# Kernel optimization log

Measured on AMD Instinct MI355X. Metric: run time of the kernel, lower is better.

The kernel has to match this reference:

```python
import jax, jax.numpy as jnp
import numpy as np

N = 50000      # total nodes
E = 600000     # edges
F_IN = 128     # dataset.num_features
G = 500        # graphs (100 nodes each)
K = 30         # sort-pool k
D1, D2, D3 = 64, 64, 1
DTOT = D1 + D2 + D3  # 129


def gcn_conv(x, W, b, src, dst, dinv, n):
    # PyG GCNConv: x' = D^-1/2 (A+I) D^-1/2 (x W) + b ; src/dst include self-loops
    h = x @ W
    norm = dinv[src] * dinv[dst]
    msg = h[src] * norm[:, None]
    return jax.ops.segment_sum(msg, dst, num_segments=n) + b


def setup_inputs():
    key = jax.random.key(0)
    ks = jax.random.split(key, 24)
    rn = lambda k, s, sc=0.1: jax.random.normal(k, s, dtype=jnp.float32) * sc
    return {
        "x": jax.random.normal(ks[0], (N, F_IN), dtype=jnp.float32),
        "edge_index": jax.random.randint(ks[1], (2, E), 0, N),
        "W1": rn(ks[2], (F_IN, D1)), "b1": rn(ks[3], (D1,)),
        "W2": rn(ks[4], (D1, D2)),  "b2": rn(ks[5], (D2,)),
        "W3": rn(ks[6], (D2, D3)),  "b3": rn(ks[7], (D3,)),
        "Ws1": rn(ks[8], (D1, 1)),  "bs1": rn(ks[9], (1,)),
        "Ws2": rn(ks[10], (D2, 1)), "bs2": rn(ks[11], (1,)),
        "Ws3": rn(ks[12], (D3, 1)), "bs3": rn(ks[13], (1,)),
        "Wc1": rn(ks[14], (16, 1, DTOT)), "bc1": rn(ks[15], (16,)),
        "Wc2": rn(ks[16], (32, 16, 5)),   "bc2": rn(ks[17], (32,)),
        "Wl1": rn(ks[18], (128, 352)),    "bl1": rn(ks[19], (128,)),
        "Wl2": rn(ks[20], (1, 128)),      "bl2": rn(ks[21], (1,)),
        "num_graphs": G,
    }


def reference(x, edge_index, W1, b1, W2, b2, W3, b3, Ws1, bs1, Ws2, bs2, Ws3, bs3,
              Wc1, bc1, Wc2, bc2, Wl1, bl1, Wl2, bl2, num_graphs):
    n = x.shape[0]
    loops = jnp.arange(n)
    src = jnp.concatenate([edge_index[0], loops])
    dst = jnp.concatenate([edge_index[1], loops])
    deg = jnp.zeros((n,), jnp.float32).at[dst].add(1.0)
    dinv = jnp.where(deg > 0, deg ** -0.5, 0.0)

    h = jax.nn.relu(gcn_conv(x, W1, b1, src, dst, dinv, n))
    x1 = gcn_conv(h, Ws1, bs1, src, dst, dinv, n) * h
    h = jax.nn.relu(gcn_conv(h, W2, b2, src, dst, dinv, n))
    x2 = gcn_conv(h, Ws2, bs2, src, dst, dinv, n) * h
    h = jax.nn.relu(gcn_conv(h, W3, b3, src, dst, dinv, n))
    x3 = gcn_conv(h, Ws3, bs3, src, dst, dinv, n) * h
    feats = jnp.concatenate([x1, x2, x3], axis=1)  # [N, 129]

    # global_sort_pool: equal-size graphs (batch = id // npg), sort desc by last channel, keep top-K
    npg = n // num_graphs
    fg = feats.reshape(num_graphs, npg, DTOT)
    order = jnp.argsort(-fg[:, :, -1], axis=1)[:, :K]                 # [G, K]
    pooled = jnp.take_along_axis(fg, order[:, :, None], axis=1)       # [G, K, 129]

    # Conv1d(1->16, kernel=129, stride=129) == per-position dense over the 129-dim blocks
    c1 = jax.nn.relu(jnp.einsum('gkd,cd->gck', pooled, Wc1[:, 0, :]) + bc1[None, :, None])  # [G,16,30]
    mp = c1.reshape(num_graphs, 16, K // 2, 2).max(axis=-1)           # MaxPool1d(2,2) -> [G,16,15]
    c2 = jax.lax.conv_general_dilated(mp, Wc2, window_strides=(1,), padding='VALID',
                                      dimension_numbers=('NCH', 'OIH', 'NCH')) + bc2[None, :, None]
    c2 = jax.nn.relu(c2)                                              # [G,32,11]
    flat = c2.reshape(num_graphs, -1)                                 # [G,352]
    hdd = jax.nn.relu(flat @ Wl1.T + bl1)
    out = hdd @ Wl2.T + bl2
    return out[:, 0]
```

## Files before the change

kernel.cpp:

```cpp
#include <hip/hip_runtime.h>
#include <hip/hip_bf16.h>

#define NN 50000
#define EE 600000
#define FIN 128
#define GG 500
#define NPG 100
#define KK 30
#define SCHUNK 1024

__global__ void psg_deg(const int* __restrict__ dst, int* __restrict__ deg, int e) {
    int i = blockIdx.x * blockDim.x + threadIdx.x;
    if (i < e) atomicAdd(&deg[dst[i]], 1);
}

__global__ __launch_bounds__(SCHUNK) void psg_scan1(const int* __restrict__ deg,
                                                    int* __restrict__ rowptr,
                                                    int* __restrict__ csums,
                                                    float* __restrict__ dinv, int n) {
    __shared__ int sm[SCHUNK];
    int t = threadIdx.x;
    int base = blockIdx.x * SCHUNK;
    int v = (base + t < n) ? deg[base + t] : 0;
    sm[t] = v;
    __syncthreads();
    for (int off = 1; off < SCHUNK; off <<= 1) {
        int u = (t >= off) ? sm[t - off] : 0;
        __syncthreads();
        sm[t] += u;
        __syncthreads();
    }
    if (base + t < n) {
        rowptr[base + t] = sm[t] - v;
        dinv[base + t] = 1.0f / sqrtf((float)(v + 1));
    }
    if (t == SCHUNK - 1) csums[blockIdx.x] = sm[t];
}

__global__ void psg_scan2(int* __restrict__ csums, int nb) {
    int t = threadIdx.x;
    int v = (t < nb) ? csums[t] : 0;
    int x = v;
#pragma unroll
    for (int off = 1; off < 64; off <<= 1) {
        int u = __shfl_up(x, off, 64);
        if (t >= off) x += u;
    }
    if (t < nb) csums[t] = x - v;
}

__global__ __launch_bounds__(SCHUNK) void psg_scan3(int* __restrict__ rowptr,
                                                    int* __restrict__ rowfill,
                                                    const int* __restrict__ csums,
                                                    int n, int e) {
    int i = blockIdx.x * SCHUNK + threadIdx.x;
    if (i < n) {
        int v = rowptr[i] + csums[blockIdx.x];
        rowptr[i] = v;
        rowfill[i] = v;
    }
    if (i == 0) rowptr[n] = e;
}

__global__ void psg_build(const int* __restrict__ src, const int* __restrict__ dst,
                          int* __restrict__ rowfill, int* __restrict__ csr_src, int e) {
    int i = blockIdx.x * blockDim.x + threadIdx.x;
    if (i < e) {
        int pos = atomicAdd(&rowfill[dst[i]], 1);
        csr_src[pos] = src[i];
    }
}

template <int KD>
__global__ __launch_bounds__(256) void psg_gemm(const float* __restrict__ X,
                                                const float* __restrict__ W,
                                                const float* __restrict__ dinv,
                                                float* __restrict__ hs, int n) {
    __shared__ __align__(16) float Xl[16][KD];
    __shared__ __align__(16) float WtF[(KD / 4) * 64 * 4];
    int t = threadIdx.x;
    int r0 = blockIdx.x * 16;
    for (int i = t; i < KD * 64; i += 256) {
        int k = i >> 6, j = i & 63;
        WtF[(((k >> 2) * 64 + j) << 2) + (k & 3)] = W[i];
    }
    for (int i4 = t; i4 < 16 * (KD / 4); i4 += 256) {
        int r = i4 / (KD / 4), u = i4 % (KD / 4);
        int row = r0 + r;
        float4 v = make_float4(0.f, 0.f, 0.f, 0.f);
        if (row < n) v = ((const float4*)(X + (size_t)row * KD))[u];
        ((float4*)&Xl[r][0])[u] = v;
    }
    __syncthreads();
    int j = t & 63, q = t >> 6;
    const float4* Wt4 = (const float4*)WtF;
    float a0 = 0.f, a1 = 0.f, a2 = 0.f, a3 = 0.f;
#pragma unroll 4
    for (int u = 0; u < KD / 4; ++u) {
        float4 wv = Wt4[u * 64 + j];
        float4 x0 = *(const float4*)&Xl[q * 4 + 0][u * 4];
        float4 x1 = *(const float4*)&Xl[q * 4 + 1][u * 4];
        float4 x2 = *(const float4*)&Xl[q * 4 + 2][u * 4];
        float4 x3 = *(const float4*)&Xl[q * 4 + 3][u * 4];
        a0 += x0.x * wv.x + x0.y * wv.y + x0.z * wv.z + x0.w * wv.w;
        a1 += x1.x * wv.x + x1.y * wv.y + x1.z * wv.z + x1.w * wv.w;
        a2 += x2.x * wv.x + x2.y * wv.y + x2.z * wv.z + x2.w * wv.w;
        a3 += x3.x * wv.x + x3.y * wv.y + x3.z * wv.z + x3.w * wv.w;
    }
    float av[4] = {a0, a1, a2, a3};
#pragma unroll
    for (int rr = 0; rr < 4; rr++) {
        int row = r0 + q * 4 + rr;
        if (row < n) hs[(size_t)row * 64 + j] = av[rr] * dinv[row];
    }
}

template <int NDOT>
__global__ __launch_bounds__(256) void psg_gfin(const float* __restrict__ hs,
                                                const int* __restrict__ rowptr,
                                                const int* __restrict__ csr_src,
                                                const float* __restrict__ dinv,
                                                const float* __restrict__ b,
                                                float* __restrict__ h,
                                                const float* __restrict__ wv0,
                                                float* __restrict__ s0_src,
                                                const float* __restrict__ wv1,
                                                float* __restrict__ s1_src, int n) {
    int w = (int)((blockIdx.x * 256 + threadIdx.x) >> 6);
    int j = threadIdx.x & 63;
    if (w >= n) return;
    int p0 = rowptr[w], p1 = rowptr[w + 1];
    float a0 = hs[(size_t)w * 64 + j];
    float a1 = 0.f, a2 = 0.f, a3 = 0.f;
    int p = p0;
    for (; p + 4 <= p1; p += 4) {
        int s0 = csr_src[p], s1 = csr_src[p + 1], s2 = csr_src[p + 2], s3 = csr_src[p + 3];
        a0 += hs[(size_t)s0 * 64 + j];
        a1 += hs[(size_t)s1 * 64 + j];
        a2 += hs[(size_t)s2 * 64 + j];
        a3 += hs[(size_t)s3 * 64 + j];
    }
    for (; p < p1; ++p) a1 += hs[(size_t)csr_src[p] * 64 + j];
    float a = (a0 + a1) + (a2 + a3);
    float di = dinv[w];
    float v = fmaxf(a * di + b[j], 0.f);
    h[(size_t)w * 64 + j] = v;
    float t0 = v * wv0[j];
#pragma unroll
    for (int o = 32; o; o >>= 1) t0 += __shfl_xor(t0, o, 64);
    if (j == 0) s0_src[w] = t0 * di;
    if (NDOT == 2) {
        float t1 = v * wv1[j];
#pragma unroll
        for (int o = 32; o; o >>= 1) t1 += __shfl_xor(t1, o, 64);
        if (j == 0) s1_src[w] = t1 * di;
    }
}

__global__ __launch_bounds__(256) void psg_sgx(const float* __restrict__ s_src,
                                               const int* __restrict__ rowptr,
                                               const int* __restrict__ csr_src,
                                               const float* __restrict__ dinv,
                                               const float* __restrict__ bs,
                                               const float* __restrict__ h,
                                               float* __restrict__ xout, int n) {
    int w = (int)((blockIdx.x * 256 + threadIdx.x) >> 6);
    int j = threadIdx.x & 63;
    if (w >= n) return;
    int p0 = rowptr[w], p1 = rowptr[w + 1];
    float part = (j == 63) ? s_src[w] : 0.f;
    for (int p = p0 + j; p < p1; p += 64) part += s_src[csr_src[p]];
#pragma unroll
    for (int o = 32; o; o >>= 1) part += __shfl_xor(part, o, 64);
    xout[(size_t)w * 64 + j] = (part * dinv[w] + bs[0]) * h[(size_t)w * 64 + j];
}

__global__ void psg_h3g(const float* __restrict__ sc_src,
                        const int* __restrict__ rowptr, const int* __restrict__ csr_src,
                        const float* __restrict__ dinv, const float* __restrict__ b3,
                        const float* __restrict__ Ws3,
                        float* __restrict__ h3, float* __restrict__ u_src, int n) {
    int i = blockIdx.x * blockDim.x + threadIdx.x;
    if (i < n) {
        float a = sc_src[i];
        int p1 = rowptr[i + 1];
        for (int p = rowptr[i]; p < p1; ++p) a += sc_src[csr_src[p]];
        float di = dinv[i];
        float v = fmaxf(a * di + b3[0], 0.f);
        h3[i] = v;
        u_src[i] = v * Ws3[0] * di;
    }
}

__device__ __forceinline__ int psg_f2ord(float f) {
    int s = __float_as_int(f);
    return s < 0 ? (s ^ 0x7fffffff) : s;
}

__global__ __launch_bounds__(128) void psg_sortpool(const float* __restrict__ u_src,
                                                    const int* __restrict__ rowptr,
                                                    const int* __restrict__ csr_src,
                                                    const float* __restrict__ dinv,
                                                    const float* __restrict__ bs3,
                                                    const float* __restrict__ h3,
                                                    const float* __restrict__ x1,
                                                    const float* __restrict__ x2,
                                                    float* __restrict__ pooled) {
    int g = blockIdx.x, t = threadIdx.x;
    __shared__ float key[NPG];
    __shared__ int ord[NPG];
    __shared__ int sel[KK];
    if (t < NPG) {
        int node = g * NPG + t;
        float a = u_src[node];
        int p1 = rowptr[node + 1];
        for (int p = rowptr[node]; p < p1; ++p) a += u_src[csr_src[p]];
        float v = (a * dinv[node] + bs3[0]) * h3[node];
        key[t] = v;
        ord[t] = psg_f2ord(v);
    }
    __syncthreads();
    if (t < NPG) {
        int v = ord[t];
        int r = 0;
        for (int m = 0; m < NPG; m++) {
            int u = ord[m];
            r += (u > v) || (u == v && m < t);
        }
        if (r < KK) sel[r] = t;
    }
    __syncthreads();
    for (int r = 0; r < KK; r++) {
        int loc = sel[r];
        int node = g * NPG + loc;
        size_t base = ((size_t)g * KK + r) * 129;
        if (t < 64) pooled[base + t] = x1[(size_t)node * 64 + t];
        else if (t < 128) pooled[base + t] = x2[(size_t)node * 64 + (t - 64)];
        if (t == 0) pooled[base + 128] = key[loc];
    }
}

__global__ __launch_bounds__(128) void psg_cnn(const float* __restrict__ pooled,
                                               const float* __restrict__ Wc1, const float* __restrict__ bc1,
                                               const float* __restrict__ Wc2, const float* __restrict__ bc2,
                                               const float* __restrict__ Wl1, const float* __restrict__ bl1,
                                               const float* __restrict__ Wl2, const float* __restrict__ bl2,
                                               float* __restrict__ out) {
    int g = blockIdx.x, t = threadIdx.x;
    __shared__ float pl[KK * 129];
    __shared__ float wc1[16 * 129];
    __shared__ float wc2[32 * 16 * 5];
    __shared__ float c1[16 * KK];
    __shared__ float mp[16 * 15];
    __shared__ float c2s[352];
    __shared__ float hdds[128];
    __shared__ float red[2];
    for (int i = t; i < KK * 129; i += 128) pl[i] = pooled[(size_t)g * KK * 129 + i];
    for (int i = t; i < 16 * 129; i += 128) wc1[i] = Wc1[i];
    for (int i = t; i < 32 * 16 * 5; i += 128) wc2[i] = Wc2[i];
    __syncthreads();
    for (int idx = t; idx < 16 * KK; idx += 128) {
        int c = idx / KK, k = idx % KK;
        float a = bc1[c];
        for (int d = 0; d < 129; d++) a += pl[k * 129 + d] * wc1[c * 129 + d];
        c1[c * KK + k] = fmaxf(a, 0.f);
    }
    __syncthreads();
    for (int idx = t; idx < 16 * 15; idx += 128) {
        int c = idx / 15, k = idx % 15;
        mp[idx] = fmaxf(c1[c * KK + 2 * k], c1[c * KK + 2 * k + 1]);
    }
    __syncthreads();
    for (int idx = t; idx < 352; idx += 128) {
        int o = idx / 11, k = idx % 11;
        float a = bc2[o];
        for (int i2 = 0; i2 < 16; i2++) {
#pragma unroll
            for (int k2 = 0; k2 < 5; k2++) a += mp[i2 * 15 + k + k2] * wc2[(o * 16 + i2) * 5 + k2];
        }
        c2s[o * 11 + k] = fmaxf(a, 0.f);
    }
    __syncthreads();
    {
        float a = bl1[t];
        const float* wr = Wl1 + (size_t)t * 352;
        for (int f = 0; f < 352; f++) a += c2s[f] * wr[f];
        hdds[t] = fmaxf(a, 0.f);
    }
    __syncthreads();
    float p = hdds[t] * Wl2[t];
#pragma unroll
    for (int o = 32; o; o >>= 1) p += __shfl_xor(p, o, 64);
    if ((t & 63) == 0) red[t >> 6] = p;
    __syncthreads();
    if (t == 0) out[g] = red[0] + red[1] + bl2[0];
}

extern "C" void kernel_launch(void* const* d_in, const int* in_sizes, int n_in,
                              void* d_out, int out_size, void* d_ws, size_t ws_size,
                              hipStream_t stream) {
    const float* x   = (const float*)d_in[0];
    const int*   ei  = (const int*)d_in[1];
    const float* W1  = (const float*)d_in[2];
    const float* b1  = (const float*)d_in[3];
    const float* W2  = (const float*)d_in[4];
    const float* b2  = (const float*)d_in[5];
    const float* W3  = (const float*)d_in[6];
    const float* b3  = (const float*)d_in[7];
    const float* Ws1 = (const float*)d_in[8];
    const float* bs1 = (const float*)d_in[9];
    const float* Ws2 = (const float*)d_in[10];
    const float* bs2 = (const float*)d_in[11];
    const float* Ws3 = (const float*)d_in[12];
    const float* bs3 = (const float*)d_in[13];
    const float* Wc1 = (const float*)d_in[14];
    const float* bc1 = (const float*)d_in[15];
    const float* Wc2 = (const float*)d_in[16];
    const float* bc2 = (const float*)d_in[17];
    const float* Wl1 = (const float*)d_in[18];
    const float* bl1 = (const float*)d_in[19];
    const float* Wl2 = (const float*)d_in[20];
    const float* bl2 = (const float*)d_in[21];
    float* out = (float*)d_out;

    const int n = in_sizes[0] / FIN;
    const int e = in_sizes[1] / 2;
    const int* src = ei;
    const int* dst = ei + e;
    const int nchunk = (n + SCHUNK - 1) / SCHUNK;

    char* w = (char*)d_ws;
    float* dinv    = (float*)w; w += (size_t)n * 4;
    float* sA_src  = (float*)w; w += (size_t)n * 4;
    float* sB_src  = (float*)w; w += (size_t)n * 4;
    float* sC_src  = (float*)w; w += (size_t)n * 4;
    float* h3      = (float*)w; w += (size_t)n * 4;
    float* u_src   = (float*)w; w += (size_t)n * 4;
    int*   deg     = (int*)w;   w += (size_t)n * 4;
    int*   rowptr  = (int*)w;   w += (size_t)(n + 1) * 4;
    int*   rowfill = (int*)w;   w += (size_t)n * 4;
    int*   csums   = (int*)w;   w += 64 * 4;
    int*   csr_src = (int*)w;   w += (size_t)e * 4;
    float* hs      = (float*)w; w += (size_t)n * 64 * 4;
    float* h1      = (float*)w; w += (size_t)n * 64 * 4;
    float* h2      = (float*)w; w += (size_t)n * 64 * 4;
    float* x1      = (float*)w; w += (size_t)n * 64 * 4;
    float* x2      = (float*)w; w += (size_t)n * 64 * 4;
    float* pooled  = (float*)w; w += (size_t)GG * KK * 129 * 4;

    const int nb_e  = (e + 255) / 256;
    const int nb_n  = (n + 255) / 256;
    const int nb_g  = (n + 15) / 16;
    const int nb_nw = (n * 64 + 255) / 256;

    hipMemsetAsync(deg, 0, (size_t)n * 4, stream);
    psg_deg<<<nb_e, 256, 0, stream>>>(dst, deg, e);
    psg_scan1<<<nchunk, SCHUNK, 0, stream>>>(deg, rowptr, csums, dinv, n);
    psg_scan2<<<1, 64, 0, stream>>>(csums, nchunk);
    psg_scan3<<<nchunk, SCHUNK, 0, stream>>>(rowptr, rowfill, csums, n, e);
    psg_build<<<nb_e, 256, 0, stream>>>(src, dst, rowfill, csr_src, e);

    psg_gemm<128><<<nb_g, 256, 0, stream>>>(x, W1, dinv, hs, n);
    psg_gfin<1><<<nb_nw, 256, 0, stream>>>(hs, rowptr, csr_src, dinv, b1, h1,
                                           Ws1, sA_src, nullptr, nullptr, n);
    psg_sgx<<<nb_nw, 256, 0, stream>>>(sA_src, rowptr, csr_src, dinv, bs1, h1, x1, n);

    psg_gemm<64><<<nb_g, 256, 0, stream>>>(h1, W2, dinv, hs, n);
    psg_gfin<2><<<nb_nw, 256, 0, stream>>>(hs, rowptr, csr_src, dinv, b2, h2,
                                           Ws2, sB_src, W3, sC_src, n);
    psg_sgx<<<nb_nw, 256, 0, stream>>>(sB_src, rowptr, csr_src, dinv, bs2, h2, x2, n);

    psg_h3g<<<nb_n, 256, 0, stream>>>(sC_src, rowptr, csr_src, dinv, b3, Ws3, h3, u_src, n);

    psg_sortpool<<<GG, 128, 0, stream>>>(u_src, rowptr, csr_src, dinv, bs3, h3, x1, x2, pooled);
    psg_cnn<<<GG, 128, 0, stream>>>(pooled, Wc1, bc1, Wc2, bc2, Wl1, bl1, Wl2, bl2, out);

    (void)n_in; (void)out_size; (void)ws_size;
}
```

Baseline: 371.0 us.

## Compute x1/x2 only for top-K pooled nodes inside sortpool; unroll gather by 8

Removes the two full-graph psg_sgx kernels that materialised x1 and x2 for all 50000 nodes. The sortpool kernel now computes the scalar GCN aggregation only for the 30 selected nodes per graph and scales h1/h2 on the fly while writing pooled. This drops two launches and large N×64 read/write passes, at the cost of a small serial neighbor loop in sortpool. The gfin aggregation loop is also unrolled to 8 independent accumulators for more memory-level parallelism.

```diff
diff --git a/kernel.cpp b/kernel.cpp
--- a/kernel.cpp
+++ b/kernel.cpp
@@ -131,17 +131,30 @@
     if (w >= n) return;
     int p0 = rowptr[w], p1 = rowptr[w + 1];
     float a0 = hs[(size_t)w * 64 + j];
-    float a1 = 0.f, a2 = 0.f, a3 = 0.f;
+    float a1 = 0.f, a2 = 0.f, a3 = 0.f, a4 = 0.f, a5 = 0.f, a6 = 0.f, a7 = 0.f;
     int p = p0;
-    for (; p + 4 <= p1; p += 4) {
-        int s0 = csr_src[p], s1 = csr_src[p + 1], s2 = csr_src[p + 2], s3 = csr_src[p + 3];
+    for (; p + 8 <= p1; p += 8) {
+        int s0 = csr_src[p],     s1 = csr_src[p + 1], s2 = csr_src[p + 2], s3 = csr_src[p + 3];
+        int s4 = csr_src[p + 4], s5 = csr_src[p + 5], s6 = csr_src[p + 6], s7 = csr_src[p + 7];
         a0 += hs[(size_t)s0 * 64 + j];
         a1 += hs[(size_t)s1 * 64 + j];
         a2 += hs[(size_t)s2 * 64 + j];
         a3 += hs[(size_t)s3 * 64 + j];
+        a4 += hs[(size_t)s4 * 64 + j];
+        a5 += hs[(size_t)s5 * 64 + j];
+        a6 += hs[(size_t)s6 * 64 + j];
+        a7 += hs[(size_t)s7 * 64 + j];
+    }
+    if (p + 4 <= p1) {
+        int s0 = csr_src[p], s1 = csr_src[p + 1], s2 = csr_src[p + 2], s3 = csr_src[p + 3];
+        a4 += hs[(size_t)s0 * 64 + j];
+        a5 += hs[(size_t)s1 * 64 + j];
+        a6 += hs[(size_t)s2 * 64 + j];
+        a7 += hs[(size_t)s3 * 64 + j];
+        p += 4;
     }
     for (; p < p1; ++p) a1 += hs[(size_t)csr_src[p] * 64 + j];
-    float a = (a0 + a1) + (a2 + a3);
+    float a = ((a0 + a1) + (a2 + a3)) + ((a4 + a5) + (a6 + a7));
     float di = dinv[w];
     float v = fmaxf(a * di + b[j], 0.f);
     h[(size_t)w * 64 + j] = v;
@@ -155,24 +168,6 @@
         for (int o = 32; o; o >>= 1) t1 += __shfl_xor(t1, o, 64);
         if (j == 0) s1_src[w] = t1 * di;
     }
-}
-
-__global__ __launch_bounds__(256) void psg_sgx(const float* __restrict__ s_src,
-                                               const int* __restrict__ rowptr,
-                                               const int* __restrict__ csr_src,
-                                               const float* __restrict__ dinv,
-                                               const float* __restrict__ bs,
-                                               const float* __restrict__ h,
-                                               float* __restrict__ xout, int n) {
-    int w = (int)((blockIdx.x * 256 + threadIdx.x) >> 6);
-    int j = threadIdx.x & 63;
-    if (w >= n) return;
-    int p0 = rowptr[w], p1 = rowptr[w + 1];
-    float part = (j == 63) ? s_src[w] : 0.f;
-    for (int p = p0 + j; p < p1; p += 64) part += s_src[csr_src[p]];
-#pragma unroll
-    for (int o = 32; o; o >>= 1) part += __shfl_xor(part, o, 64);
-    xout[(size_t)w * 64 + j] = (part * dinv[w] + bs[0]) * h[(size_t)w * 64 + j];
 }
 
 __global__ void psg_h3g(const float* __restrict__ sc_src,
@@ -201,20 +196,25 @@
                                                     const int* __restrict__ rowptr,
                                                     const int* __restrict__ csr_src,
                                                     const float* __restrict__ dinv,
+                                                    const float* __restrict__ bs1,
+                                                    const float* __restrict__ bs2,
                                                     const float* __restrict__ bs3,
+                                                    const float* __restrict__ sA_src,
+                                                    const float* __restrict__ sB_src,
+                                                    const float* __restrict__ h1,
+                                                    const float* __restrict__ h2,
                                                     const float* __restrict__ h3,
-                                                    const float* __restrict__ x1,
-                                                    const float* __restrict__ x2,
                                                     float* __restrict__ pooled) {
     int g = blockIdx.x, t = threadIdx.x;
     __shared__ float key[NPG];
     __shared__ int ord[NPG];
     __shared__ int sel[KK];
+    __shared__ float sa[KK], sb[KK];
     if (t < NPG) {
         int node = g * NPG + t;
         float a = u_src[node];
-        int p1 = rowptr[node + 1];
-        for (int p = rowptr[node]; p < p1; ++p) a += u_src[csr_src[p]];
+        int pe = rowptr[node + 1];
+        for (int p = rowptr[node]; p < pe; ++p) a += u_src[csr_src[p]];
         float v = (a * dinv[node] + bs3[0]) * h3[node];
         key[t] = v;
         ord[t] = psg_f2ord(v);
@@ -230,13 +230,27 @@
         if (r < KK) sel[r] = t;
     }
     __syncthreads();
-    for (int r = 0; r < KK; r++) {
-        int loc = sel[r];
-        int node = g * NPG + loc;
-        size_t base = ((size_t)g * KK + r) * 129;
-        if (t < 64) pooled[base + t] = x1[(size_t)node * 64 + t];
-        else if (t < 128) pooled[base + t] = x2[(size_t)node * 64 + (t - 64)];
-        if (t == 0) pooled[base + 128] = key[loc];
+    {
+        int r = t & 31;
+        if (t < 64 && r < KK) {
+            int node = g * NPG + sel[r];
+            const float* ssrc = (t < 32) ? sA_src : sB_src;
+            float a = ssrc[node];
+            int pe = rowptr[node + 1];
+            for (int p = rowptr[node]; p < pe; ++p) a += ssrc[csr_src[p]];
+            float scl = a * dinv[node] + ((t < 32) ? bs1[0] : bs2[0]);
+            if (t < 32) sa[r] = scl; else sb[r] = scl;
+        }
+    }
+    __syncthreads();
+    for (int idx = t; idx < KK * 129; idx += 128) {
+        int r = idx / 129, c = idx - r * 129;
+        int node = g * NPG + sel[r];
+        float v;
+        if (c < 64) v = sa[r] * h1[(size_t)node * 64 + c];
+        else if (c < 128) v = sb[r] * h2[(size_t)node * 64 + (c - 64)];
+        else v = key[sel[r]];
+        pooled[((size_t)g * KK + r) * 129 + c] = v;
     }
 }
 
@@ -344,8 +358,6 @@
     float* hs      = (float*)w; w += (size_t)n * 64 * 4;
     float* h1      = (float*)w; w += (size_t)n * 64 * 4;
     float* h2      = (float*)w; w += (size_t)n * 64 * 4;
-    float* x1      = (float*)w; w += (size_t)n * 64 * 4;
-    float* x2      = (float*)w; w += (size_t)n * 64 * 4;
     float* pooled  = (float*)w; w += (size_t)GG * KK * 129 * 4;
 
     const int nb_e  = (e + 255) / 256;
@@ -363,16 +375,15 @@
     psg_gemm<128><<<nb_g, 256, 0, stream>>>(x, W1, dinv, hs, n);
     psg_gfin<1><<<nb_nw, 256, 0, stream>>>(hs, rowptr, csr_src, dinv, b1, h1,
                                            Ws1, sA_src, nullptr, nullptr, n);
-    psg_sgx<<<nb_nw, 256, 0, stream>>>(sA_src, rowptr, csr_src, dinv, bs1, h1, x1, n);
 
     psg_gemm<64><<<nb_g, 256, 0, stream>>>(h1, W2, dinv, hs, n);
     psg_gfin<2><<<nb_nw, 256, 0, stream>>>(hs, rowptr, csr_src, dinv, b2, h2,
                                            Ws2, sB_src, W3, sC_src, n);
-    psg_sgx<<<nb_nw, 256, 0, stream>>>(sB_src, rowptr, csr_src, dinv, bs2, h2, x2, n);
 
     psg_h3g<<<nb_n, 256, 0, stream>>>(sC_src, rowptr, csr_src, dinv, b3, Ws3, h3, u_src, n);
 
-    psg_sortpool<<<GG, 128, 0, stream>>>(u_src, rowptr, csr_src, dinv, bs3, h3, x1, x2, pooled);
+    psg_sortpool<<<GG, 128, 0, stream>>>(u_src, rowptr, csr_src, dinv, bs1, bs2, bs3,
+                                         sA_src, sB_src, h1, h2, h3, pooled);
     psg_cnn<<<GG, 128, 0, stream>>>(pooled, Wc1, bc1, Wc2, bc2, Wl1, bl1, Wl2, bl2, out);
 
     (void)n_in; (void)out_size; (void)ws_size;
```

New measurement: 355.0 us. -4.3%, faster.
